# Optimization experiments

Measured on AMD Instinct MI355X. Metric: run time of the kernel, lower is better.

Reference implementation:

```python
import jax, jax.numpy as jnp
import numpy as np

B, L, H = 512, 1000, 128


def _lstm_cell(x_t, h, c, w_ih, w_hh, b_ih, b_hh):
    # PyTorch LSTMCell: gates = x @ W_ih^T + b_ih + h @ W_hh^T + b_hh, gate order i,f,g,o
    gates = x_t @ w_ih.T + b_ih + h @ w_hh.T + b_hh  # [B, 4H]
    i, f, g, o = jnp.split(gates, 4, axis=-1)
    i = jax.nn.sigmoid(i)
    f = jax.nn.sigmoid(f)
    g = jnp.tanh(g)
    o = jax.nn.sigmoid(o)
    c_new = f * c + i * g
    h_new = o * jnp.tanh(c_new)
    return h_new, c_new


def setup_inputs() -> dict:
    key = jax.random.key(0)
    ks = jax.random.split(key, 12)
    s = 1.0 / np.sqrt(H)  # torch default uniform(-1/sqrt(H), 1/sqrt(H))
    u = lambda k, shp: jax.random.uniform(k, shp, jnp.float32, -s, s)
    return {
        "x": jax.random.normal(ks[0], (B, L), jnp.float32),
        "w_ih1": u(ks[1], (4 * H, 1)),
        "w_hh1": u(ks[2], (4 * H, H)),
        "b_ih1": u(ks[3], (4 * H,)),
        "b_hh1": u(ks[4], (4 * H,)),
        "w_ih2": u(ks[5], (4 * H, H)),
        "w_hh2": u(ks[6], (4 * H, H)),
        "b_ih2": u(ks[7], (4 * H,)),
        "b_hh2": u(ks[8], (4 * H,)),
        "w_lin": u(ks[9], (1, H)),
        "b_lin": u(ks[10], (1,)),
    }


def reference(x, w_ih1, w_hh1, b_ih1, b_hh1, w_ih2, w_hh2, b_ih2, b_hh2, w_lin, b_lin):
    n = x.shape[0]
    h = w_hh1.shape[1]
    zeros = jnp.zeros((n, h), x.dtype)
    init = (zeros, zeros, zeros, zeros)  # h1, c1, h2, c2

    def step(carry, x_t):
        h1, c1, h2, c2 = carry
        h1, c1 = _lstm_cell(x_t, h1, c1, w_ih1, w_hh1, b_ih1, b_hh1)
        h2, c2 = _lstm_cell(h1, h2, c2, w_ih2, w_hh2, b_ih2, b_hh2)
        out = h2 @ w_lin.T + b_lin  # [B, 1]
        return (h1, c1, h2, c2), out[:, 0]

    xs = x.T[:, :, None]  # [L, B, 1]
    _, outs = jax.lax.scan(step, init, xs)  # outs: [L, B]
    return outs.T  # [B, L]
```

## Files before the change

### kernel.cpp

```cpp
#include <hip/hip_runtime.h>

#define B_ 512
#define L_ 1000
#define H_ 128
#define G_ 512

typedef _Float16 v8h __attribute__((ext_vector_type(8)));
typedef float v4f __attribute__((ext_vector_type(4)));

__device__ __forceinline__ float sigmoid_f(float x) {
  return __builtin_amdgcn_rcpf(1.0f + __builtin_amdgcn_exp2f(-1.4426950408889634f * x));
}
__device__ __forceinline__ float tanh_f(float x) {
  return 1.0f - 2.0f * __builtin_amdgcn_rcpf(1.0f + __builtin_amdgcn_exp2f(2.8853900817779268f * x));
}
__device__ __forceinline__ float sel4(v4f v, int j) {
  float lo = (j & 1) ? v[1] : v[0];
  float hi = (j & 1) ? v[3] : v[2];
  return (j & 2) ? hi : lo;
}

#define FB_KT 144

#define MFMA16(a, b, c) __builtin_amdgcn_mfma_f32_16x16x32_f16((a), (b), (c), 0, 0, 0)

__global__ __launch_bounds__(512, 2) void lstm_mfma(
    const float* __restrict__ x,
    const float* __restrict__ w_ih1,
    const float* __restrict__ w_hh1,
    const float* __restrict__ b_ih1,
    const float* __restrict__ b_hh1,
    const float* __restrict__ w_ih2,
    const float* __restrict__ w_hh2,
    const float* __restrict__ b_ih2,
    const float* __restrict__ b_hh2,
    const float* __restrict__ w_lin,
    const float* __restrict__ b_lin,
    float* __restrict__ out)
{
  __shared__ __align__(16) float xlds[2][L_];
  __shared__ __align__(16) float olds[2 * L_];
  __shared__ __align__(16) unsigned char hb1[2][4 * FB_KT];
  __shared__ __align__(16) unsigned char hb2[2][4 * FB_KT];
  __shared__ __align__(16) float bbb1[G_];
  __shared__ __align__(16) float bbb2[G_];

  const int tid  = threadIdx.x;
  const int wv   = tid >> 6;
  const int lane = tid & 63;
  const int quad = lane >> 4;
  const int m15  = lane & 15;
  const int r0   = blockIdx.x * 2;

  for (int i = tid; i < 2 * L_; i += 512) {
    ((float*)xlds)[i] = x[r0 * L_ + i];
    olds[i] = 0.f;
  }
  bbb1[tid] = b_ih1[tid] + b_hh1[tid];
  bbb2[tid] = b_ih2[tid] + b_hh2[tid];
  if (tid < 288) {
    ((unsigned*)hb1)[tid] = 0u;
    ((unsigned*)hb2)[tid] = 0u;
  }
  const float blv = b_lin[0];

  const int jsel = (m15 >> 1) & 3;
  const int rsel = m15 & 1;
  const int esel = 16 * wv + 4 * quad + jsel;
  const float wxi_s = w_ih1[esel];
  const float wxf_s = w_ih1[128 + esel];
  const float wxg_s = w_ih1[256 + esel];
  const float wxo_s = w_ih1[384 + esel];
  const float wl_s  = w_lin[esel];
  const int hwo1 = (wv >> 1) * FB_KT + (2 * (wv & 1) + (quad >> 1)) * 32
                 + rsel * 16 + (4 * (quad & 1) + jsel) * 2;

  v8h A1f[4][4], A2if[4][4], A2hf[4][4];
#pragma unroll
  for (int m = 0; m < 4; ++m) {
    const int grow = ((wv + 8 * m) * 16 + m15) * H_;
#pragma unroll
    for (int kt = 0; kt < 4; ++kt) {
      const int koff = kt * 32 + quad * 8;
      float4 a, b;
      a = *(const float4*)(w_hh1 + grow + koff);
      b = *(const float4*)(w_hh1 + grow + koff + 4);
      A1f[m][kt] = v8h{(_Float16)a.x, (_Float16)a.y, (_Float16)a.z, (_Float16)a.w,
                       (_Float16)b.x, (_Float16)b.y, (_Float16)b.z, (_Float16)b.w};
      a = *(const float4*)(w_ih2 + grow + koff);
      b = *(const float4*)(w_ih2 + grow + koff + 4);
      A2if[m][kt] = v8h{(_Float16)a.x, (_Float16)a.y, (_Float16)a.z, (_Float16)a.w,
                        (_Float16)b.x, (_Float16)b.y, (_Float16)b.z, (_Float16)b.w};
      a = *(const float4*)(w_hh2 + grow + koff);
      b = *(const float4*)(w_hh2 + grow + koff + 4);
      A2hf[m][kt] = v8h{(_Float16)a.x, (_Float16)a.y, (_Float16)a.z, (_Float16)a.w,
                        (_Float16)b.x, (_Float16)b.y, (_Float16)b.z, (_Float16)b.w};
    }
  }

  float c1 = 0.f, c2 = 0.f;

  const int cbase = 16 * wv + 4 * quad;
  const int roff  = quad * 32 + (m15 & 1) * 16;

  __syncthreads();

  for (int t = 0; t < L_; ++t) {
    v4f a0 = *(const v4f*)&bbb1[cbase];
    v4f a1 = *(const v4f*)&bbb1[128 + cbase];
    v4f a2 = *(const v4f*)&bbb1[256 + cbase];
    v4f a3 = *(const v4f*)&bbb1[384 + cbase];
    {
      const unsigned char* bp = &hb1[(t + 1) & 1][0];
      __builtin_amdgcn_s_setprio(1);
#pragma unroll
      for (int kt = 0; kt < 4; ++kt) {
        v8h b = *(const v8h*)(bp + kt * FB_KT + roff);
        a0 = MFMA16(A1f[0][kt], b, a0);
        a1 = MFMA16(A1f[1][kt], b, a1);
        a2 = MFMA16(A1f[2][kt], b, a2);
        a3 = MFMA16(A1f[3][kt], b, a3);
      }
      __builtin_amdgcn_s_setprio(0);
    }
    {
      const float xv = xlds[rsel][t];
      float iv = sigmoid_f(sel4(a0, jsel) + wxi_s * xv);
      float fv = sigmoid_f(sel4(a1, jsel) + wxf_s * xv);
      float gv = tanh_f(sel4(a2, jsel) + wxg_s * xv);
      float ov = sigmoid_f(sel4(a3, jsel) + wxo_s * xv);
      c1 = fv * c1 + iv * gv;
      float h = ov * tanh_f(c1);
      if (m15 < 8) *(_Float16*)(&hb1[t & 1][0] + hwo1) = (_Float16)h;
    }
    __syncthreads();

    v4f d0 = *(const v4f*)&bbb2[cbase];
    v4f d1 = *(const v4f*)&bbb2[128 + cbase];
    v4f d2 = *(const v4f*)&bbb2[256 + cbase];
    v4f d3 = *(const v4f*)&bbb2[384 + cbase];
    {
      const unsigned char* p1 = &hb1[t & 1][0];
      const unsigned char* p2 = &hb2[(t + 1) & 1][0];
      __builtin_amdgcn_s_setprio(1);
#pragma unroll
      for (int kt = 0; kt < 4; ++kt) {
        v8h b1 = *(const v8h*)(p1 + kt * FB_KT + roff);
        v8h b2 = *(const v8h*)(p2 + kt * FB_KT + roff);
        d0 = MFMA16(A2if[0][kt], b1, d0);
        d1 = MFMA16(A2if[1][kt], b1, d1);
        d2 = MFMA16(A2if[2][kt], b1, d2);
        d3 = MFMA16(A2if[3][kt], b1, d3);
        d0 = MFMA16(A2hf[0][kt], b2, d0);
        d1 = MFMA16(A2hf[1][kt], b2, d1);
        d2 = MFMA16(A2hf[2][kt], b2, d2);
        d3 = MFMA16(A2hf[3][kt], b2, d3);
      }
      __builtin_amdgcn_s_setprio(0);
    }
    {
      float iv = sigmoid_f(sel4(d0, jsel));
      float fv = sigmoid_f(sel4(d1, jsel));
      float gv = tanh_f(sel4(d2, jsel));
      float ov = sigmoid_f(sel4(d3, jsel));
      c2 = fv * c2 + iv * gv;
      float h = ov * tanh_f(c2);
      if (m15 < 8) *(_Float16*)(&hb2[t & 1][0] + hwo1) = (_Float16)h;
      float p = (m15 < 8) ? h * wl_s : 0.f;
      p += __shfl_xor(p, 2, 64);
      p += __shfl_xor(p, 4, 64);
      p += __shfl_xor(p, 16, 64);
      p += __shfl_xor(p, 32, 64);
      if (lane < 2) atomicAdd(&olds[lane * L_ + t], p);
    }
    __syncthreads();
  }

  for (int i = tid; i < 2 * L_; i += 512) out[r0 * L_ + i] = olds[i] + blv;
}

extern "C" void kernel_launch(void* const* d_in, const int* in_sizes, int n_in,
                              void* d_out, int out_size, void* d_ws, size_t ws_size,
                              hipStream_t stream) {
  const float* x     = (const float*)d_in[0];
  const float* w_ih1 = (const float*)d_in[1];
  const float* w_hh1 = (const float*)d_in[2];
  const float* b_ih1 = (const float*)d_in[3];
  const float* b_hh1 = (const float*)d_in[4];
  const float* w_ih2 = (const float*)d_in[5];
  const float* w_hh2 = (const float*)d_in[6];
  const float* b_ih2 = (const float*)d_in[7];
  const float* b_hh2 = (const float*)d_in[8];
  const float* w_lin = (const float*)d_in[9];
  const float* b_lin = (const float*)d_in[10];

  lstm_mfma<<<B_ / 2, 512, 0, stream>>>(
      x, w_ih1, w_hh1, b_ih1, b_hh1, w_ih2, w_hh2, b_ih2, b_hh2,
      w_lin, b_lin, (float*)d_out);
}
```

Measured before the change: 1.414 ms.

## Skew layer-1 and layer-2 LSTM steps to share one barrier per timestep

Software-pipelines the two LSTM layers so iteration s computes layer 2 at step s and layer 1 at step s+1 together. Both read the same h1 buffer, so one __syncthreads replaces two per step, and the two layers' MFMA chains can overlap. A prologue computes the first layer-1 step from biases alone. This costs more live registers for the two accumulator sets and depends on the double-buffer indexing being right.

Measured after the change: 1.811 ms. 28.0% more time.

```diff
diff --git a/kernel.cpp b/kernel.cpp
--- a/kernel.cpp
+++ b/kernel.cpp
@@ -105,59 +105,53 @@
 
   __syncthreads();
 
-  for (int t = 0; t < L_; ++t) {
+  {
+    const float xv = xlds[rsel][0];
+    float iv = sigmoid_f(bbb1[esel] + wxi_s * xv);
+    float fv = sigmoid_f(bbb1[128 + esel] + wxf_s * xv);
+    float gv = tanh_f(bbb1[256 + esel] + wxg_s * xv);
+    float ov = sigmoid_f(bbb1[384 + esel] + wxo_s * xv);
+    c1 = iv * gv;
+    float h = ov * tanh_f(c1);
+    if (m15 < 8) *(_Float16*)(&hb1[0][0] + hwo1) = (_Float16)h;
+  }
+  __syncthreads();
+
+  for (int s = 0; s < L_; ++s) {
+    v4f d0 = *(const v4f*)&bbb2[cbase];
+    v4f d1 = *(const v4f*)&bbb2[128 + cbase];
+    v4f d2 = *(const v4f*)&bbb2[256 + cbase];
+    v4f d3 = *(const v4f*)&bbb2[384 + cbase];
+    const unsigned char* p1 = &hb1[s & 1][0];
+    const unsigned char* p2 = &hb2[(s + 1) & 1][0];
+    __builtin_amdgcn_s_setprio(1);
+#pragma unroll
+    for (int kt = 0; kt < 4; ++kt) {
+      v8h b1 = *(const v8h*)(p1 + kt * FB_KT + roff);
+      v8h b2 = *(const v8h*)(p2 + kt * FB_KT + roff);
+      d0 = MFMA16(A2if[0][kt], b1, d0);
+      d1 = MFMA16(A2if[1][kt], b1, d1);
+      d2 = MFMA16(A2if[2][kt], b1, d2);
+      d3 = MFMA16(A2if[3][kt], b1, d3);
+      d0 = MFMA16(A2hf[0][kt], b2, d0);
+      d1 = MFMA16(A2hf[1][kt], b2, d1);
+      d2 = MFMA16(A2hf[2][kt], b2, d2);
+      d3 = MFMA16(A2hf[3][kt], b2, d3);
+    }
     v4f a0 = *(const v4f*)&bbb1[cbase];
     v4f a1 = *(const v4f*)&bbb1[128 + cbase];
     v4f a2 = *(const v4f*)&bbb1[256 + cbase];
     v4f a3 = *(const v4f*)&bbb1[384 + cbase];
-    {
-      const unsigned char* bp = &hb1[(t + 1) & 1][0];
-      __builtin_amdgcn_s_setprio(1);
-#pragma unroll
-      for (int kt = 0; kt < 4; ++kt) {
-        v8h b = *(const v8h*)(bp + kt * FB_KT + roff);
-        a0 = MFMA16(A1f[0][kt], b, a0);
-        a1 = MFMA16(A1f[1][kt], b, a1);
-        a2 = MFMA16(A1f[2][kt], b, a2);
-        a3 = MFMA16(A1f[3][kt], b, a3);
-      }
-      __builtin_amdgcn_s_setprio(0);
-    }
-    {
-      const float xv = xlds[rsel][t];
-      float iv = sigmoid_f(sel4(a0, jsel) + wxi_s * xv);
-      float fv = sigmoid_f(sel4(a1, jsel) + wxf_s * xv);
-      float gv = tanh_f(sel4(a2, jsel) + wxg_s * xv);
-      float ov = sigmoid_f(sel4(a3, jsel) + wxo_s * xv);
-      c1 = fv * c1 + iv * gv;
-      float h = ov * tanh_f(c1);
-      if (m15 < 8) *(_Float16*)(&hb1[t & 1][0] + hwo1) = (_Float16)h;
-    }
-    __syncthreads();
-
-    v4f d0 = *(const v4f*)&bbb2[cbase];
-    v4f d1 = *(const v4f*)&bbb2[128 + cbase];
-    v4f d2 = *(const v4f*)&bbb2[256 + cbase];
-    v4f d3 = *(const v4f*)&bbb2[384 + cbase];
-    {
-      const unsigned char* p1 = &hb1[t & 1][0];
-      const unsigned char* p2 = &hb2[(t + 1) & 1][0];
-      __builtin_amdgcn_s_setprio(1);
-#pragma unroll
-      for (int kt = 0; kt < 4; ++kt) {
-        v8h b1 = *(const v8h*)(p1 + kt * FB_KT + roff);
-        v8h b2 = *(const v8h*)(p2 + kt * FB_KT + roff);
-        d0 = MFMA16(A2if[0][kt], b1, d0);
-        d1 = MFMA16(A2if[1][kt], b1, d1);
-        d2 = MFMA16(A2if[2][kt], b1, d2);
-        d3 = MFMA16(A2if[3][kt], b1, d3);
-        d0 = MFMA16(A2hf[0][kt], b2, d0);
-        d1 = MFMA16(A2hf[1][kt], b2, d1);
-        d2 = MFMA16(A2hf[2][kt], b2, d2);
-        d3 = MFMA16(A2hf[3][kt], b2, d3);
-      }
-      __builtin_amdgcn_s_setprio(0);
-    }
+#pragma unroll
+    for (int kt = 0; kt < 4; ++kt) {
+      v8h b1 = *(const v8h*)(p1 + kt * FB_KT + roff);
+      a0 = MFMA16(A1f[0][kt], b1, a0);
+      a1 = MFMA16(A1f[1][kt], b1, a1);
+      a2 = MFMA16(A1f[2][kt], b1, a2);
+      a3 = MFMA16(A1f[3][kt], b1, a3);
+    }
+    __builtin_amdgcn_s_setprio(0);
+
     {
       float iv = sigmoid_f(sel4(d0, jsel));
       float fv = sigmoid_f(sel4(d1, jsel));
@@ -165,13 +159,23 @@
       float ov = sigmoid_f(sel4(d3, jsel));
       c2 = fv * c2 + iv * gv;
       float h = ov * tanh_f(c2);
-      if (m15 < 8) *(_Float16*)(&hb2[t & 1][0] + hwo1) = (_Float16)h;
+      if (m15 < 8) *(_Float16*)(&hb2[s & 1][0] + hwo1) = (_Float16)h;
       float p = (m15 < 8) ? h * wl_s : 0.f;
       p += __shfl_xor(p, 2, 64);
       p += __shfl_xor(p, 4, 64);
       p += __shfl_xor(p, 16, 64);
       p += __shfl_xor(p, 32, 64);
-      if (lane < 2) atomicAdd(&olds[lane * L_ + t], p);
+      if (lane < 2) atomicAdd(&olds[lane * L_ + s], p);
+    }
+    if (s + 1 < L_) {
+      const float xv = xlds[rsel][s + 1];
+      float iv = sigmoid_f(sel4(a0, jsel) + wxi_s * xv);
+      float fv = sigmoid_f(sel4(a1, jsel) + wxf_s * xv);
+      float gv = tanh_f(sel4(a2, jsel) + wxg_s * xv);
+      float ov = sigmoid_f(sel4(a3, jsel) + wxo_s * xv);
+      c1 = fv * c1 + iv * gv;
+      float h = ov * tanh_f(c1);
+      if (m15 < 8) *(_Float16*)(&hb1[(s + 1) & 1][0] + hwo1) = (_Float16)h;
     }
     __syncthreads();
   }
```
